# Optimization experiments

Measured on AMD Instinct MI355X. Metric: run time of the kernel, lower is better.

The kernel has to match this reference:

```python
import jax, jax.numpy as jnp
import numpy as np

HIDDEN = 2048
N_HEADS = 16
N_KV_HEADS = 4
HEAD_DIM = HIDDEN // N_HEADS  # 128
N_GROUPS = N_HEADS // N_KV_HEADS  # 4


def rotate_half(x):
    # interleaved rotate: (-x_odd, x_even) interleaved back
    x_even = x[..., ::2]
    x_odd = x[..., 1::2]
    return jnp.stack((-x_odd, x_even), axis=-1).reshape(x.shape)


def setup_inputs() -> dict:
    key = jax.random.key(0)
    ks = jax.random.split(key, 8)
    B, S = 4, 2048
    x = jax.random.normal(ks[0], (B, S, HIDDEN), dtype=jnp.float32)
    # RoPE tables (precomputed cos/sin over max positions)
    inv_freq = 1.0 / (1000000.0 ** (np.arange(0, HEAD_DIM, 2, dtype=np.float32) / HEAD_DIM))
    t = np.arange(S, dtype=np.float32)
    freqs = np.outer(t, inv_freq)  # [S, HEAD_DIM/2]
    emb = np.repeat(freqs, 2, axis=-1)  # interleaved layout [S, HEAD_DIM]
    cos = jnp.asarray(np.cos(emb))
    sin = jnp.asarray(np.sin(emb))
    scale = 0.02
    Wq = jax.random.normal(ks[1], (HIDDEN, N_HEADS * HEAD_DIM), dtype=jnp.float32) * scale
    Wk = jax.random.normal(ks[2], (HIDDEN, N_KV_HEADS * HEAD_DIM), dtype=jnp.float32) * scale
    Wv = jax.random.normal(ks[3], (HIDDEN, N_KV_HEADS * HEAD_DIM), dtype=jnp.float32) * scale
    Wo = jax.random.normal(ks[4], (N_HEADS * HEAD_DIM, HIDDEN), dtype=jnp.float32) * scale
    return {"x": x, "cos": cos, "sin": sin, "Wq": Wq, "Wk": Wk, "Wv": Wv, "Wo": Wo}


def reference(x, cos, sin, Wq, Wk, Wv, Wo):
    B, S, D = x.shape
    q = (x @ Wq).reshape(B, S, N_HEADS, HEAD_DIM).transpose(0, 2, 1, 3)      # [B,H,S,d]
    k = (x @ Wk).reshape(B, S, N_KV_HEADS, HEAD_DIM).transpose(0, 2, 1, 3)   # [B,Hkv,S,d]
    v = (x @ Wv).reshape(B, S, N_KV_HEADS, HEAD_DIM).transpose(0, 2, 1, 3)
    # RoPE: position_ids = arange(S); cos/sin [S,d] -> [1,1,S,d]
    c = cos[:S][None, None, :, :]
    s = sin[:S][None, None, :, :]
    q = q * c + rotate_half(q) * s
    k = k * c + rotate_half(k) * s
    # repeat_kv: [B,Hkv,S,d] -> [B,H,S,d]
    k = jnp.repeat(k, N_GROUPS, axis=1)
    v = jnp.repeat(v, N_GROUPS, axis=1)
    # causal SDPA
    scores = jnp.einsum("bhqd,bhkd->bhqk", q, k) / jnp.sqrt(jnp.float32(HEAD_DIM))
    neg = jnp.finfo(scores.dtype).min
    causal = jnp.triu(jnp.full((S, S), neg, dtype=scores.dtype), k=1)
    scores = scores + causal[None, None]
    attn = jax.nn.softmax(scores.astype(jnp.float32), axis=-1).astype(q.dtype)
    out = jnp.einsum("bhqk,bhkd->bhqd", attn, v)
    out = out.transpose(0, 2, 1, 3).reshape(B, S, N_HEADS * HEAD_DIM)
    return out @ Wo
```

## Files before the change

kernel.cpp:

```cpp
#include <hip/hip_runtime.h>
#include <stdint.h>

#define S_LEN 2048
#define BATCH 4
#define HID   2048
#define HD    128
#define NKV   4
#define MTOT  (BATCH*S_LEN)
#define NQT2  (S_LEN/256)
#define QSCALE 0.08838834764831845f

typedef float    f32x4  __attribute__((ext_vector_type(4)));
typedef __bf16   bf16x8 __attribute__((ext_vector_type(8)));
typedef __bf16   bf16x4 __attribute__((ext_vector_type(4)));
typedef unsigned u32x2  __attribute__((ext_vector_type(2)));

__device__ __forceinline__ void gld16(const void* g, void* l) {
    __builtin_amdgcn_global_load_lds(
        (const __attribute__((address_space(1))) void*)g,
        (__attribute__((address_space(3))) void*)l, 16, 0, 0);
}

__global__ void k_conv_x(const float* __restrict__ in, __bf16* __restrict__ out) {
    int i = blockIdx.x * blockDim.x + threadIdx.x;
    f32x4 a = ((const f32x4*)in)[2 * i];
    f32x4 b = ((const f32x4*)in)[2 * i + 1];
    bf16x8 o;
    o[0] = (__bf16)a[0]; o[1] = (__bf16)a[1]; o[2] = (__bf16)a[2]; o[3] = (__bf16)a[3];
    o[4] = (__bf16)b[0]; o[5] = (__bf16)b[1]; o[6] = (__bf16)b[2]; o[7] = (__bf16)b[3];
    ((bf16x8*)out)[i] = o;
}

__global__ void k_transpose_all(const float* __restrict__ Wq,
                                const float* __restrict__ Wk,
                                const float* __restrict__ Wv,
                                const float* __restrict__ Wo,
                                __bf16* __restrict__ wqt,
                                __bf16* __restrict__ wkvt,
                                __bf16* __restrict__ wot) {
    const int z = blockIdx.z;
    const float* in; __bf16* out; int N;
    if      (z == 0) { in = Wq; out = wqt;  N = 2048; }
    else if (z == 1) { in = Wk; out = wkvt; N = 512;  }
    else if (z == 2) { in = Wv; out = wkvt + (size_t)512 * HID; N = 512; }
    else             { in = Wo; out = wot;  N = 2048; }
    int k0 = blockIdx.x * 64, n0 = blockIdx.y * 64;
    if (n0 >= N) return;
    __shared__ float tile[64][65];
    for (int e = threadIdx.x; e < 4096; e += 256) {
        int r = e >> 6, c = e & 63;
        tile[r][c] = in[(size_t)(k0 + r) * N + n0 + c];
    }
    __syncthreads();
    for (int e = threadIdx.x; e < 4096; e += 256) {
        int r = e >> 6, c = e & 63;
        out[(size_t)(n0 + r) * HID + k0 + c] = (__bf16)tile[c][r];
    }
}

__global__ __launch_bounds__(256) void k_gemm_qkv(const __bf16* __restrict__ A,
                                                  const __bf16* __restrict__ Bt,
                                                  unsigned char* __restrict__ qb8,
                                                  unsigned char* __restrict__ kb8,
                                                  __bf16* __restrict__ vtb,
                                                  const float* __restrict__ cosp,
                                                  const float* __restrict__ sinp) {
    __shared__ __align__(16) char smem[33792];
    __bf16* As = (__bf16*)smem;
    __bf16* Bs = (__bf16*)(smem + 16384);
    const int tid = threadIdx.x, lane = tid & 63, wave = tid >> 6;
    const int wm = wave >> 1, wn = wave & 1;
    const int id = blockIdx.x;
    const int xcd = id & 7, g = id >> 3;
    const int m0 = (xcd * 8 + (g & 7)) * 128;
    const int n0 = (g >> 3) * 128;
    const int lo = lane & 15, hi = lane >> 4;
    f32x4 acc[4][4] = {};

    const int srow = wave * 8 + (lane >> 3);
    const int sp   = lane & 7;

    for (int kt = 0; kt < HID; kt += 64) {
#pragma unroll
        for (int r = 0; r < 4; r++) {
            int row = r * 32 + srow;
            int c = sp ^ (row & 7);
            gld16(A + (size_t)(m0 + row) * HID + kt + c * 8, &As[(r * 32 + wave * 8) * 64]);
        }
#pragma unroll
        for (int r = 0; r < 4; r++) {
            int row = r * 32 + srow;
            int c = sp ^ (row & 7);
            gld16(Bt + (size_t)(n0 + row) * HID + kt + c * 8, &Bs[(r * 32 + wave * 8) * 64]);
        }
        __syncthreads();
#pragma unroll
        for (int ks = 0; ks < 2; ks++) {
            bf16x8 af[4], bfr[4];
#pragma unroll
            for (int mt = 0; mt < 4; mt++) {
                int row = wm * 64 + mt * 16 + lo;
                int pp = (ks * 4 + hi) ^ (row & 7);
                af[mt] = *(const bf16x8*)&As[row * 64 + pp * 8];
            }
#pragma unroll
            for (int nt = 0; nt < 4; nt++) {
                int row = wn * 64 + nt * 16 + lo;
                int pp = (ks * 4 + hi) ^ (row & 7);
                bfr[nt] = *(const bf16x8*)&Bs[row * 64 + pp * 8];
            }
#pragma unroll
            for (int mt = 0; mt < 4; mt++)
#pragma unroll
                for (int nt = 0; nt < 4; nt++)
                    acc[mt][nt] = __builtin_amdgcn_mfma_f32_16x16x32_bf16(
                        af[mt], bfr[nt], acc[mt][nt], 0, 0, 0);
        }
        __syncthreads();
    }

    if (n0 < 2560) {
        __bf16* Cs = (__bf16*)smem;
#pragma unroll
        for (int mt = 0; mt < 4; mt++)
#pragma unroll
            for (int nt = 0; nt < 4; nt++) {
                int rl = wm * 64 + mt * 16 + hi * 4;
                int cl = wn * 64 + nt * 16 + lo;
#pragma unroll
                for (int r = 0; r < 4; r++)
                    Cs[(rl + r) * 132 + cl] = (__bf16)acc[mt][nt][r];
            }
        __syncthreads();

        const int crow = tid >> 4;
        const int cch  = tid & 15;
        const int colg = n0 + cch * 8;
        const bool isQ = n0 < 2048;
        const int d0 = colg & (HD - 1);
#pragma unroll
        for (int rep = 0; rep < 8; rep++) {
            int row = rep * 16 + crow;
            int rowg = m0 + row;
            bf16x8 v = *(const bf16x8*)&Cs[row * 132 + cch * 8];
            float f[8];
#pragma unroll
            for (int j = 0; j < 8; j++) f[j] = (float)v[j];
            {
                int s = rowg & (S_LEN - 1);
                f32x4 c0 = *(const f32x4*)&cosp[s * HD + d0];
                f32x4 c1 = *(const f32x4*)&cosp[s * HD + d0 + 4];
                f32x4 s0 = *(const f32x4*)&sinp[s * HD + d0];
                f32x4 s1 = *(const f32x4*)&sinp[s * HD + d0 + 4];
                float cc[8] = {c0[0], c0[1], c0[2], c0[3], c1[0], c1[1], c1[2], c1[3]};
                float ss[8] = {s0[0], s0[1], s0[2], s0[3], s1[0], s1[1], s1[2], s1[3]};
#pragma unroll
                for (int p = 0; p < 4; p++) {
                    float e0 = f[2 * p], e1 = f[2 * p + 1];
                    f[2 * p]     = e0 * cc[2 * p]     - e1 * ss[2 * p];
                    f[2 * p + 1] = e1 * cc[2 * p + 1] + e0 * ss[2 * p + 1];
                }
            }
            if (isQ) {
#pragma unroll
                for (int j = 0; j < 8; j++) f[j] *= QSCALE;
            }
            int u0 = __builtin_amdgcn_cvt_pk_fp8_f32(f[0], f[1], 0, false);
            u0     = __builtin_amdgcn_cvt_pk_fp8_f32(f[2], f[3], u0, true);
            int u1 = __builtin_amdgcn_cvt_pk_fp8_f32(f[4], f[5], 0, false);
            u1     = __builtin_amdgcn_cvt_pk_fp8_f32(f[6], f[7], u1, true);
            u32x2 pk; pk[0] = (unsigned)u0; pk[1] = (unsigned)u1;
            if (isQ) *(u32x2*)&qb8[(size_t)rowg * HID + colg] = pk;
            else     *(u32x2*)&kb8[(size_t)rowg * 512 + (colg - 2048)] = pk;
        }
    } else {
        __bf16* CsT = (__bf16*)smem;
#pragma unroll
        for (int mt = 0; mt < 4; mt++)
#pragma unroll
            for (int nt = 0; nt < 4; nt++) {
                int cl = wn * 64 + nt * 16 + lo;
                int mrow = wm * 64 + mt * 16 + hi * 4;
                bf16x4 w;
#pragma unroll
                for (int r = 0; r < 4; r++) w[r] = (__bf16)acc[mt][nt][r];
                *(bf16x4*)&CsT[cl * 132 + mrow] = w;
            }
        __syncthreads();

        const int kvh = (n0 - 2560) >> 7;
        const int bb = m0 >> 11;
        const int s0 = m0 & (S_LEN - 1);
        __bf16* dst = vtb + (size_t)(bb * NKV + kvh) * HD * S_LEN;
        const int dloc = tid >> 4;
        const int sch  = tid & 15;
#pragma unroll
        for (int rep = 0; rep < 8; rep++) {
            int d = rep * 16 + dloc;
            bf16x8 v = *(const bf16x8*)&CsT[d * 132 + sch * 8];
            *(bf16x8*)&dst[(size_t)d * S_LEN + s0 + sch * 8] = v;
        }
    }
}

__global__ __launch_bounds__(256) void k_gemm_o(const __bf16* __restrict__ A,
                                                const __bf16* __restrict__ Bt,
                                                float* __restrict__ Cp) {
    __shared__ __bf16 As[128 * 64];
    __shared__ __bf16 Bs[128 * 64];
    const int tid = threadIdx.x, lane = tid & 63, wave = tid >> 6;
    const int wm = wave >> 1, wn = wave & 1;
    const int id = blockIdx.x;
    const int xcd = id & 7, g = id >> 3;
    const int m0 = (xcd * 8 + (g & 7)) * 128;
    const int n0 = (g >> 3) * 128;
    const int lo = lane & 15, hi = lane >> 4;
    f32x4 acc[4][4] = {};

    const int srow = wave * 8 + (lane >> 3);
    const int sp   = lane & 7;

    for (int kt = 0; kt < HID; kt += 64) {
#pragma unroll
        for (int r = 0; r < 4; r++) {
            int row = r * 32 + srow;
            int c = sp ^ (row & 7);
            gld16(A + (size_t)(m0 + row) * HID + kt + c * 8, &As[(r * 32 + wave * 8) * 64]);
        }
#pragma unroll
        for (int r = 0; r < 4; r++) {
            int row = r * 32 + srow;
            int c = sp ^ (row & 7);
            gld16(Bt + (size_t)(n0 + row) * HID + kt + c * 8, &Bs[(r * 32 + wave * 8) * 64]);
        }
        __syncthreads();
#pragma unroll
        for (int ks = 0; ks < 2; ks++) {
            bf16x8 af[4], bfr[4];
#pragma unroll
            for (int mt = 0; mt < 4; mt++) {
                int row = wm * 64 + mt * 16 + lo;
                int pp = (ks * 4 + hi) ^ (row & 7);
                af[mt] = *(const bf16x8*)&As[row * 64 + pp * 8];
            }
#pragma unroll
            for (int nt = 0; nt < 4; nt++) {
                int row = wn * 64 + nt * 16 + lo;
                int pp = (ks * 4 + hi) ^ (row & 7);
                bfr[nt] = *(const bf16x8*)&Bs[row * 64 + pp * 8];
            }
#pragma unroll
            for (int mt = 0; mt < 4; mt++)
#pragma unroll
                for (int nt = 0; nt < 4; nt++)
                    acc[mt][nt] = __builtin_amdgcn_mfma_f32_16x16x32_bf16(
                        af[mt], bfr[nt], acc[mt][nt], 0, 0, 0);
        }
        __syncthreads();
    }
#pragma unroll
    for (int mt = 0; mt < 4; mt++) {
#pragma unroll
        for (int nt = 0; nt < 4; nt++) {
            int row = m0 + wm * 64 + mt * 16 + hi * 4;
            int col = n0 + wn * 64 + nt * 16 + lo;
#pragma unroll
            for (int r = 0; r < 4; r++)
                Cp[(size_t)(row + r) * HID + col] = acc[mt][nt][r];
        }
    }
}

__global__ __launch_bounds__(512) void k_attn(const unsigned char* __restrict__ qb8,
                                              const unsigned char* __restrict__ kb8,
                                              const __bf16* __restrict__ vtb,
                                              __bf16* __restrict__ ob) {
    __shared__ char   Ks8[2][64 * 128];
    __shared__ __bf16 Vs[2][128 * 64];
    __shared__ __bf16 Ps[8][2048];
    const int tid = threadIdx.x, lane = tid & 63, wave = tid >> 6;
    const int pair = blockIdx.x, h = blockIdx.y, b = blockIdx.z;
    const int kvh = h >> 2;
    const int lo = lane & 15, hi = lane >> 4;
    char* PsW = (char*)&Ps[wave][0];

    const unsigned char* kbb = kb8 + (size_t)b * S_LEN * 512 + kvh * HD;
    const __bf16* vbb = vtb + (size_t)(b * NKV + kvh) * HD * S_LEN;

    const int krow_s = tid >> 3;
    const int kp_s   = tid & 7;
    const int vrow_s = wave * 8 + (lane >> 3);
    const int vp_s   = lane & 7;

    auto STAGE_K = [&](int buf, int t) {
        int c = kp_s ^ (krow_s & 7);
        gld16(kbb + (size_t)(t * 64 + krow_s) * 512 + c * 16,
              &Ks8[buf][wave * 1024]);
    };
    auto STAGE_V = [&](int buf, int t) {
#pragma unroll
        for (int r = 0; r < 2; r++) {
            int row = r * 64 + vrow_s;
            int c = vp_s ^ (row & 7);
            gld16(vbb + (size_t)row * S_LEN + t * 64 + c * 8,
                  &Vs[buf][(r * 64 + wave * 8) * 64]);
        }
    };

    auto SM = [&](f32x4 (&sc)[4], float& Mr, float& Lr, f32x4 (&o)[8]) {
        float mloc = sc[0][0];
#pragma unroll
        for (int nt = 0; nt < 4; nt++)
#pragma unroll
            for (int r = 0; r < 4; r++) mloc = fmaxf(mloc, sc[nt][r]);
        mloc = fmaxf(mloc, __shfl_xor(mloc, 16, 64));
        mloc = fmaxf(mloc, __shfl_xor(mloc, 32, 64));
        float mn = (mloc <= Mr + 8.f) ? Mr : mloc;
        float sum = 0.f;
#pragma unroll
        for (int nt = 0; nt < 4; nt++)
#pragma unroll
            for (int r = 0; r < 4; r++) {
                float e = __expf(sc[nt][r] - mn);
                sc[nt][r] = e;
                sum += e;
            }
        sum += __shfl_xor(sum, 16, 64);
        sum += __shfl_xor(sum, 32, 64);
        if (mn != Mr) {
            float scl = __expf(Mr - mn);
            Lr = Lr * scl + sum;
            Mr = mn;
#pragma unroll
            for (int dt = 0; dt < 8; dt++) o[dt] *= scl;
        } else {
            Lr += sum;
        }
    };

#pragma unroll 1
    for (int pi = 0; pi < 2; pi++) {
        const int qt = pi ? (NQT2 - 1 - pair) : pair;
        const int nkv = 4 * qt + 4;
        const int qbase = qt * 256 + wave * 32;

        const unsigned char* qp0 = qb8 + (size_t)(b * S_LEN + qbase + lo) * HID + h * HD;
        const unsigned char* qp1 = qp0 + (size_t)16 * HID;
        long qa0[4], qa1[4];
#pragma unroll
        for (int kf = 0; kf < 4; kf++) {
            qa0[kf] = *(const long*)(qp0 + kf * 32 + hi * 8);
            qa1[kf] = *(const long*)(qp1 + kf * 32 + hi * 8);
        }

        f32x4 o0[8] = {}, o1[8] = {};
        float Mr0 = -3e30f, Lr0 = 0.f, Mr1 = -3e30f, Lr1 = 0.f;

        int cur = 0;
        if (pi == 1) __syncthreads();
        STAGE_K(0, 0);
        STAGE_V(0, 0);
        __syncthreads();

#pragma unroll 1
        for (int t = 0; t < nkv; t++) {
            if (t < nkv - 1) { STAGE_K(cur ^ 1, t + 1); STAGE_V(cur ^ 1, t + 1); }

            f32x4 sc0[4], sc1[4];
            __builtin_amdgcn_s_setprio(1);
#pragma unroll
            for (int nt = 0; nt < 4; nt++) {
                f32x4 a = {0.f, 0.f, 0.f, 0.f}, bb = {0.f, 0.f, 0.f, 0.f};
#pragma unroll
                for (int kf = 0; kf < 4; kf++) {
                    int row = nt * 16 + lo;
                    int lch = 2 * kf + (hi >> 1);
                    long kf8 = *(const long*)&Ks8[cur][row * 128 +
                                ((lch ^ (row & 7)) * 16) + (hi & 1) * 8];
                    a  = __builtin_amdgcn_mfma_f32_16x16x32_fp8_fp8(kf8, qa0[kf], a, 0, 0, 0);
                    bb = __builtin_amdgcn_mfma_f32_16x16x32_fp8_fp8(kf8, qa1[kf], bb, 0, 0, 0);
                }
                sc0[nt] = a; sc1[nt] = bb;
            }
            __builtin_amdgcn_s_setprio(0);

            if (t * 64 + 63 > qbase) {
                int qg = qbase + lo;
#pragma unroll
                for (int nt = 0; nt < 4; nt++)
#pragma unroll
                    for (int r = 0; r < 4; r++) {
                        int kg = t * 64 + nt * 16 + hi * 4 + r;
                        if (kg > qg) sc0[nt][r] = -1e30f;
                    }
            }
            if (t * 64 + 63 > qbase + 16) {
                int qg = qbase + 16 + lo;
#pragma unroll
                for (int nt = 0; nt < 4; nt++)
#pragma unroll
                    for (int r = 0; r < 4; r++) {
                        int kg = t * 64 + nt * 16 + hi * 4 + r;
                        if (kg > qg) sc1[nt][r] = -1e30f;
                    }
            }

            SM(sc0, Mr0, Lr0, o0);
            SM(sc1, Mr1, Lr1, o1);

#pragma unroll
            for (int nt = 0; nt < 4; nt++) {
                bf16x4 p0, p1;
#pragma unroll
                for (int r = 0; r < 4; r++) { p0[r] = (__bf16)sc0[nt][r]; p1[r] = (__bf16)sc1[nt][r]; }
                int off = lo * 128 + ((nt * 32 + hi * 8) ^ ((lo & 7) << 4));
                *(bf16x4*)(PsW + off)        = p0;
                *(bf16x4*)(PsW + 2048 + off) = p1;
            }
            asm volatile("s_waitcnt lgkmcnt(0)" ::: "memory");
            bf16x8 pf0[2], pf1[2];
#pragma unroll
            for (int c = 0; c < 2; c++) {
                int off = lo * 128 + ((c * 64 + hi * 16) ^ ((lo & 7) << 4));
                pf0[c] = *(const bf16x8*)(PsW + off);
                pf1[c] = *(const bf16x8*)(PsW + 2048 + off);
            }
            __builtin_amdgcn_s_setprio(1);
#pragma unroll
            for (int dt = 0; dt < 8; dt++) {
                int rowd = dt * 16 + lo;
#pragma unroll
                for (int c = 0; c < 2; c++) {
                    int ch = c * 4 + hi;
                    bf16x8 vv = *(const bf16x8*)&Vs[cur][rowd * 64 + (ch ^ (rowd & 7)) * 8];
                    o0[dt] = __builtin_amdgcn_mfma_f32_16x16x32_bf16(vv, pf0[c], o0[dt], 0, 0, 0);
                    o1[dt] = __builtin_amdgcn_mfma_f32_16x16x32_bf16(vv, pf1[c], o1[dt], 0, 0, 0);
                }
            }
            __builtin_amdgcn_s_setprio(0);
            __syncthreads();
            cur ^= 1;
        }

        const int qe = lane >> 2, c4 = lane & 3;
#pragma unroll
        for (int sub = 0; sub < 2; sub++) {
            float rl = 1.0f / (sub ? Lr1 : Lr0);
            char* Pp = PsW + sub * 2048;
#pragma unroll
            for (int h2 = 0; h2 < 2; h2++) {
#pragma unroll
                for (int dt4 = 0; dt4 < 4; dt4++) {
                    f32x4 ov = sub ? o1[h2 * 4 + dt4] : o0[h2 * 4 + dt4];
                    bf16x4 w;
#pragma unroll
                    for (int r = 0; r < 4; r++) w[r] = (__bf16)(ov[r] * rl);
                    *(bf16x4*)(Pp + lo * 128 + ((dt4 * 32 + hi * 8) ^ ((lo & 7) << 4))) = w;
                }
                asm volatile("s_waitcnt lgkmcnt(0)" ::: "memory");
                __builtin_amdgcn_sched_barrier(0);
#pragma unroll
                for (int s2 = 0; s2 < 2; s2++) {
                    int ch = c4 + s2 * 4;
                    bf16x8 v = *(const bf16x8*)(Pp + qe * 128 + ((ch * 16) ^ ((qe & 7) << 4)));
                    int qg = qbase + sub * 16 + qe;
                    int col = h * HD + h2 * 64 + ch * 8;
                    *(bf16x8*)&ob[(size_t)(b * S_LEN + qg) * HID + col] = v;
                }
            }
        }
    }
}

extern "C" void kernel_launch(void* const* d_in, const int* in_sizes, int n_in,
                              void* d_out, int out_size, void* d_ws, size_t ws_size,
                              hipStream_t stream) {
    (void)in_sizes; (void)n_in; (void)out_size; (void)ws_size;
    const float* x    = (const float*)d_in[0];
    const float* cosp = (const float*)d_in[1];
    const float* sinp = (const float*)d_in[2];
    const float* Wq   = (const float*)d_in[3];
    const float* Wk   = (const float*)d_in[4];
    const float* Wv   = (const float*)d_in[5];
    const float* Wo   = (const float*)d_in[6];
    float* out = (float*)d_out;

    char* ws = (char*)d_ws;
    __bf16*        xb   = (__bf16*)(ws);
    __bf16*        wqt  = (__bf16*)(ws + 33554432);
    __bf16*        wkvt = (__bf16*)(ws + 41943040);
    __bf16*        wot  = (__bf16*)(ws + 46137344);
    unsigned char* qb8  = (unsigned char*)(ws + 54525952);
    unsigned char* kb8  = (unsigned char*)(ws + 71303168);
    __bf16*        vtb  = (__bf16*)(ws + 75497472);
    __bf16*        aob  = xb;

    k_conv_x<<<MTOT * HID / 8 / 256, 256, 0, stream>>>(x, xb);
    { dim3 g(32, 32, 4);
      k_transpose_all<<<g, 256, 0, stream>>>(Wq, Wk, Wv, Wo, wqt, wkvt, wot); }

    k_gemm_qkv<<<1536, 256, 0, stream>>>(xb, wqt, qb8, kb8, vtb, cosp, sinp);

    { dim3 g(NQT2 / 2, 16, BATCH); k_attn<<<g, 512, 0, stream>>>(qb8, kb8, vtb, aob); }

    k_gemm_o<<<1024, 256, 0, stream>>>(aob, wot, out);
}
```

Measured before the change: 338.2 us.

## Replace output GEMM with 256x256 double-buffered 8-wave ping-pong kernel

New measurement: 327.3 us. 3.2% less time.

```diff
diff --git a/kernel.cpp b/kernel.cpp
--- a/kernel.cpp
+++ b/kernel.cpp
@@ -203,72 +203,132 @@
     }
 }
 
-__global__ __launch_bounds__(256) void k_gemm_o(const __bf16* __restrict__ A,
-                                                const __bf16* __restrict__ Bt,
-                                                float* __restrict__ Cp) {
-    __shared__ __bf16 As[128 * 64];
-    __shared__ __bf16 Bs[128 * 64];
+#define BARM asm volatile("s_barrier" ::: "memory")
+#define BAR1 do { BARM;                                                       \
+                  asm volatile("s_waitcnt lgkmcnt(0)" ::: "memory");          \
+                  __builtin_amdgcn_sched_barrier(0); } while (0)
+#define BAR2 BARM
+#define MM(qm, qn)                                                            \
+    do {                                                                      \
+        __builtin_amdgcn_s_setprio(1);                                        \
+        _Pragma("unroll") for (int ks = 0; ks < 2; ks++)                      \
+        _Pragma("unroll") for (int mf = 0; mf < 4; mf++)                      \
+        _Pragma("unroll") for (int nf = 0; nf < 2; nf++)                      \
+            acc[qm][qn][mf][nf] = __builtin_amdgcn_mfma_f32_16x16x32_bf16(    \
+                af[mf][ks], bf[nf][ks], acc[qm][qn][mf][nf], 0, 0, 0);        \
+        __builtin_amdgcn_s_setprio(0);                                        \
+    } while (0)
+
+__global__ __launch_bounds__(512) void k_gemm_o8(const __bf16* __restrict__ A,
+                                                 const __bf16* __restrict__ Bt,
+                                                 float* __restrict__ Cp) {
+    __shared__ __bf16 Ab[2][2][128 * 64];
+    __shared__ __bf16 Bb[2][2][128 * 64];
     const int tid = threadIdx.x, lane = tid & 63, wave = tid >> 6;
-    const int wm = wave >> 1, wn = wave & 1;
-    const int id = blockIdx.x;
-    const int xcd = id & 7, g = id >> 3;
-    const int m0 = (xcd * 8 + (g & 7)) * 128;
-    const int n0 = (g >> 3) * 128;
+    const int wm = wave >> 2, wn = wave & 3;
+    const int m0 = (blockIdx.x >> 3) * 256;
+    const int n0 = (blockIdx.x & 7) * 256;
     const int lo = lane & 15, hi = lane >> 4;
-    f32x4 acc[4][4] = {};
+    f32x4 acc[2][2][4][2] = {};
 
     const int srow = wave * 8 + (lane >> 3);
     const int sp   = lane & 7;
 
-    for (int kt = 0; kt < HID; kt += 64) {
-#pragma unroll
-        for (int r = 0; r < 4; r++) {
-            int row = r * 32 + srow;
-            int c = sp ^ (row & 7);
-            gld16(A + (size_t)(m0 + row) * HID + kt + c * 8, &As[(r * 32 + wave * 8) * 64]);
-        }
-#pragma unroll
-        for (int r = 0; r < 4; r++) {
-            int row = r * 32 + srow;
-            int c = sp ^ (row & 7);
-            gld16(Bt + (size_t)(n0 + row) * HID + kt + c * 8, &Bs[(r * 32 + wave * 8) * 64]);
-        }
-        __syncthreads();
-#pragma unroll
-        for (int ks = 0; ks < 2; ks++) {
-            bf16x8 af[4], bfr[4];
-#pragma unroll
-            for (int mt = 0; mt < 4; mt++) {
-                int row = wm * 64 + mt * 16 + lo;
-                int pp = (ks * 4 + hi) ^ (row & 7);
-                af[mt] = *(const bf16x8*)&As[row * 64 + pp * 8];
-            }
-#pragma unroll
-            for (int nt = 0; nt < 4; nt++) {
-                int row = wn * 64 + nt * 16 + lo;
-                int pp = (ks * 4 + hi) ^ (row & 7);
-                bfr[nt] = *(const bf16x8*)&Bs[row * 64 + pp * 8];
-            }
-#pragma unroll
-            for (int mt = 0; mt < 4; mt++)
-#pragma unroll
-                for (int nt = 0; nt < 4; nt++)
-                    acc[mt][nt] = __builtin_amdgcn_mfma_f32_16x16x32_bf16(
-                        af[mt], bfr[nt], acc[mt][nt], 0, 0, 0);
-        }
-        __syncthreads();
+    auto STA = [&](int s, int h, int t) {
+#pragma unroll
+        for (int p = 0; p < 2; p++) {
+            int rr = p * 64 + srow;
+            int c = sp ^ (rr & 7);
+            gld16(A + (size_t)(m0 + h * 128 + rr) * HID + t * 64 + c * 8,
+                  &Ab[s][h][(p * 64 + wave * 8) * 64]);
+        }
+    };
+    auto STB = [&](int s, int h, int t) {
+#pragma unroll
+        for (int p = 0; p < 2; p++) {
+            int rr = p * 64 + srow;
+            int c = sp ^ (rr & 7);
+            gld16(Bt + (size_t)(n0 + h * 128 + rr) * HID + t * 64 + c * 8,
+                  &Bb[s][h][(p * 64 + wave * 8) * 64]);
+        }
+    };
+
+    bf16x8 af[4][2], bf[2][2];
+    auto LDA = [&](int s, int qm) {
+#pragma unroll
+        for (int mf = 0; mf < 4; mf++) {
+            int rr = wm * 64 + mf * 16 + lo;
+#pragma unroll
+            for (int ks = 0; ks < 2; ks++) {
+                int pp = (ks * 4 + hi) ^ (rr & 7);
+                af[mf][ks] = *(const bf16x8*)&Ab[s][qm][rr * 64 + pp * 8];
+            }
+        }
+    };
+    auto LDB = [&](int s, int qn) {
+#pragma unroll
+        for (int nf = 0; nf < 2; nf++) {
+            int rr = wn * 32 + nf * 16 + lo;
+#pragma unroll
+            for (int ks = 0; ks < 2; ks++) {
+                int pp = (ks * 4 + hi) ^ (rr & 7);
+                bf[nf][ks] = *(const bf16x8*)&Bb[s][qn][rr * 64 + pp * 8];
+            }
+        }
+    };
+
+    STA(0, 0, 0); STB(0, 0, 0); STA(0, 1, 0); STB(0, 1, 0);
+    STA(1, 1, 1); STB(1, 1, 1);
+    asm volatile("s_waitcnt vmcnt(4)" ::: "memory");
+    BARM;
+
+#pragma unroll 1
+    for (int i = 0; i < 16; i++) {
+        const int t0 = 2 * i, t1 = 2 * i + 1;
+        const bool more = (i < 15);
+        LDA(0, 0); LDB(0, 0);
+        STA(1, 0, t1); STB(1, 0, t1);
+        BAR1; MM(0, 0); BAR2;
+        LDB(0, 1);
+        BAR1; MM(0, 1); BAR2;
+        LDA(0, 1); LDB(0, 0);
+        if (more) STA(0, 0, t0 + 2);
+        BAR1; MM(1, 0); BAR2;
+        LDB(0, 1);
+        if (more) STB(0, 0, t0 + 2);
+        BAR1; MM(1, 1);
+        if (more) { asm volatile("s_waitcnt vmcnt(4)" ::: "memory"); }
+        else      { asm volatile("s_waitcnt vmcnt(0)" ::: "memory"); }
+        BAR2;
+        LDA(1, 1); LDB(1, 1);
+        if (more) { STA(0, 1, t0 + 2); STB(0, 1, t0 + 2); }
+        BAR1; MM(1, 1); BAR2;
+        LDB(1, 0);
+        BAR1; MM(1, 0); BAR2;
+        LDA(1, 0); LDB(1, 1);
+        if (more) STA(1, 1, t1 + 2);
+        BAR1; MM(0, 1); BAR2;
+        LDB(1, 0);
+        if (more) STB(1, 1, t1 + 2);
+        BAR1; MM(0, 0);
+        if (more) { asm volatile("s_waitcnt vmcnt(4)" ::: "memory"); }
+        BAR2;
     }
-#pragma unroll
-    for (int mt = 0; mt < 4; mt++) {
-#pragma unroll
-        for (int nt = 0; nt < 4; nt++) {
-            int row = m0 + wm * 64 + mt * 16 + hi * 4;
-            int col = n0 + wn * 64 + nt * 16 + lo;
-#pragma unroll
-            for (int r = 0; r < 4; r++)
-                Cp[(size_t)(row + r) * HID + col] = acc[mt][nt][r];
-        }
-    }
+
+#pragma unroll
+    for (int qm = 0; qm < 2; qm++)
+#pragma unroll
+        for (int qn = 0; qn < 2; qn++)
+#pragma unroll
+            for (int mf = 0; mf < 4; mf++)
+#pragma unroll
+                for (int nf = 0; nf < 2; nf++) {
+                    int row = m0 + qm * 128 + wm * 64 + mf * 16 + hi * 4;
+                    int col = n0 + qn * 128 + wn * 32 + nf * 16 + lo;
+#pragma unroll
+                    for (int r = 0; r < 4; r++)
+                        Cp[(size_t)(row + r) * HID + col] = acc[qm][qn][mf][nf][r];
+                }
 }
 
 __global__ __launch_bounds__(512) void k_attn(const unsigned char* __restrict__ qb8,
@@ -503,5 +563,5 @@
 
     { dim3 g(NQT2 / 2, 16, BATCH); k_attn<<<g, 512, 0, stream>>>(qb8, kb8, vtb, aob); }
 
-    k_gemm_o<<<1024, 256, 0, stream>>>(aob, wot, out);
-}
+    k_gemm_o8<<<256, 512, 0, stream>>>(aob, wot, out);
+}
```

## Use 256x256 double-buffered ping-pong GEMM for Q and output projections

Applied to the files above, without the earlier changes.

Result: faster. 319.2 us (-5.6%).

```diff
diff --git a/kernel.cpp b/kernel.cpp
--- a/kernel.cpp
+++ b/kernel.cpp
@@ -58,95 +58,140 @@
     }
 }
 
-__global__ __launch_bounds__(256) void k_gemm_qkv(const __bf16* __restrict__ A,
-                                                  const __bf16* __restrict__ Bt,
-                                                  unsigned char* __restrict__ qb8,
-                                                  unsigned char* __restrict__ kb8,
-                                                  __bf16* __restrict__ vtb,
-                                                  const float* __restrict__ cosp,
-                                                  const float* __restrict__ sinp) {
-    __shared__ __align__(16) char smem[33792];
-    __bf16* As = (__bf16*)smem;
-    __bf16* Bs = (__bf16*)(smem + 16384);
-    const int tid = threadIdx.x, lane = tid & 63, wave = tid >> 6;
-    const int wm = wave >> 1, wn = wave & 1;
-    const int id = blockIdx.x;
-    const int xcd = id & 7, g = id >> 3;
-    const int m0 = (xcd * 8 + (g & 7)) * 128;
-    const int n0 = (g >> 3) * 128;
-    const int lo = lane & 15, hi = lane >> 4;
-    f32x4 acc[4][4] = {};
-
-    const int srow = wave * 8 + (lane >> 3);
-    const int sp   = lane & 7;
-
-    for (int kt = 0; kt < HID; kt += 64) {
-#pragma unroll
-        for (int r = 0; r < 4; r++) {
-            int row = r * 32 + srow;
-            int c = sp ^ (row & 7);
-            gld16(A + (size_t)(m0 + row) * HID + kt + c * 8, &As[(r * 32 + wave * 8) * 64]);
-        }
-#pragma unroll
-        for (int r = 0; r < 4; r++) {
-            int row = r * 32 + srow;
-            int c = sp ^ (row & 7);
-            gld16(Bt + (size_t)(n0 + row) * HID + kt + c * 8, &Bs[(r * 32 + wave * 8) * 64]);
-        }
-        __syncthreads();
-#pragma unroll
-        for (int ks = 0; ks < 2; ks++) {
-            bf16x8 af[4], bfr[4];
-#pragma unroll
-            for (int mt = 0; mt < 4; mt++) {
-                int row = wm * 64 + mt * 16 + lo;
-                int pp = (ks * 4 + hi) ^ (row & 7);
-                af[mt] = *(const bf16x8*)&As[row * 64 + pp * 8];
-            }
-#pragma unroll
-            for (int nt = 0; nt < 4; nt++) {
-                int row = wn * 64 + nt * 16 + lo;
-                int pp = (ks * 4 + hi) ^ (row & 7);
-                bfr[nt] = *(const bf16x8*)&Bs[row * 64 + pp * 8];
-            }
-#pragma unroll
-            for (int mt = 0; mt < 4; mt++)
-#pragma unroll
-                for (int nt = 0; nt < 4; nt++)
-                    acc[mt][nt] = __builtin_amdgcn_mfma_f32_16x16x32_bf16(
-                        af[mt], bfr[nt], acc[mt][nt], 0, 0, 0);
-        }
-        __syncthreads();
+#define BARM asm volatile("s_barrier" ::: "memory")
+#define BAR1 do { BARM;                                                       \
+                  asm volatile("s_waitcnt lgkmcnt(0)" ::: "memory");          \
+                  __builtin_amdgcn_sched_barrier(0); } while (0)
+#define BAR2 BARM
+#define MM(qm, qn)                                                            \
+    do {                                                                      \
+        __builtin_amdgcn_s_setprio(1);                                        \
+        _Pragma("unroll") for (int ks = 0; ks < 2; ks++)                      \
+        _Pragma("unroll") for (int mf = 0; mf < 4; mf++)                      \
+        _Pragma("unroll") for (int nf = 0; nf < 2; nf++)                      \
+            acc[qm][qn][mf][nf] = __builtin_amdgcn_mfma_f32_16x16x32_bf16(    \
+                af[mf][ks], bf[nf][ks], acc[qm][qn][mf][nf], 0, 0, 0);        \
+        __builtin_amdgcn_s_setprio(0);                                        \
+    } while (0)
+
+#define GEMM8_BODY(Aptr, Bptr)                                                \
+    __shared__ __bf16 Ab[2][2][128 * 64];                                     \
+    __shared__ __bf16 Bb[2][2][128 * 64];                                     \
+    const int tid = threadIdx.x, lane = tid & 63, wave = tid >> 6;            \
+    const int wm = wave >> 2, wn = wave & 3;                                  \
+    const int lo = lane & 15, hi = lane >> 4;                                 \
+    f32x4 acc[2][2][4][2] = {};                                               \
+    const int srow = wave * 8 + (lane >> 3);                                  \
+    const int sp   = lane & 7;                                                \
+    auto STA = [&](int s, int h, int t) {                                     \
+        _Pragma("unroll") for (int p = 0; p < 2; p++) {                       \
+            int rr = p * 64 + srow;                                           \
+            int c = sp ^ (rr & 7);                                            \
+            gld16(Aptr + (size_t)(m0 + h * 128 + rr) * HID + t * 64 + c * 8,  \
+                  &Ab[s][h][(p * 64 + wave * 8) * 64]);                       \
+        }                                                                     \
+    };                                                                        \
+    auto STB = [&](int s, int h, int t) {                                     \
+        _Pragma("unroll") for (int p = 0; p < 2; p++) {                       \
+            int rr = p * 64 + srow;                                           \
+            int c = sp ^ (rr & 7);                                            \
+            gld16(Bptr + (size_t)(n0 + h * 128 + rr) * HID + t * 64 + c * 8,  \
+                  &Bb[s][h][(p * 64 + wave * 8) * 64]);                       \
+        }                                                                     \
+    };                                                                        \
+    bf16x8 af[4][2], bf[2][2];                                                \
+    auto LDA = [&](int s, int qm) {                                           \
+        _Pragma("unroll") for (int mf = 0; mf < 4; mf++) {                    \
+            int rr = wm * 64 + mf * 16 + lo;                                  \
+            _Pragma("unroll") for (int ks = 0; ks < 2; ks++) {                \
+                int pp = (ks * 4 + hi) ^ (rr & 7);                            \
+                af[mf][ks] = *(const bf16x8*)&Ab[s][qm][rr * 64 + pp * 8];    \
+            }                                                                 \
+        }                                                                     \
+    };                                                                        \
+    auto LDB = [&](int s, int qn) {                                           \
+        _Pragma("unroll") for (int nf = 0; nf < 2; nf++) {                    \
+            int rr = wn * 32 + nf * 16 + lo;                                  \
+            _Pragma("unroll") for (int ks = 0; ks < 2; ks++) {                \
+                int pp = (ks * 4 + hi) ^ (rr & 7);                            \
+                bf[nf][ks] = *(const bf16x8*)&Bb[s][qn][rr * 64 + pp * 8];    \
+            }                                                                 \
+        }                                                                     \
+    };                                                                        \
+    STA(0, 0, 0); STB(0, 0, 0); STA(0, 1, 0); STB(0, 1, 0);                   \
+    STA(1, 1, 1); STB(1, 1, 1);                                               \
+    asm volatile("s_waitcnt vmcnt(4)" ::: "memory");                          \
+    BARM;                                                                     \
+    _Pragma("unroll 1")                                                       \
+    for (int i = 0; i < 16; i++) {                                            \
+        const int t0 = 2 * i, t1 = 2 * i + 1;                                 \
+        const bool more = (i < 15);                                           \
+        LDA(0, 0); LDB(0, 0);                                                 \
+        STA(1, 0, t1); STB(1, 0, t1);                                         \
+        BAR1; MM(0, 0); BAR2;                                                 \
+        LDB(0, 1);                                                            \
+        BAR1; MM(0, 1); BAR2;                                                 \
+        LDA(0, 1); LDB(0, 0);                                                 \
+        if (more) STA(0, 0, t0 + 2);                                          \
+        BAR1; MM(1, 0); BAR2;                                                 \
+        LDB(0, 1);                                                            \
+        if (more) STB(0, 0, t0 + 2);                                          \
+        BAR1; MM(1, 1);                                                       \
+        if (more) { asm volatile("s_waitcnt vmcnt(4)" ::: "memory"); }        \
+        else      { asm volatile("s_waitcnt vmcnt(0)" ::: "memory"); }        \
+        BAR2;                                                                 \
+        LDA(1, 1); LDB(1, 1);                                                 \
+        if (more) { STA(0, 1, t0 + 2); STB(0, 1, t0 + 2); }                   \
+        BAR1; MM(1, 1); BAR2;                                                 \
+        LDB(1, 0);                                                            \
+        BAR1; MM(1, 0); BAR2;                                                 \
+        LDA(1, 0); LDB(1, 1);                                                 \
+        if (more) STA(1, 1, t1 + 2);                                          \
+        BAR1; MM(0, 1); BAR2;                                                 \
+        LDB(1, 0);                                                            \
+        if (more) STB(1, 1, t1 + 2);                                          \
+        BAR1; MM(0, 0);                                                       \
+        if (more) { asm volatile("s_waitcnt vmcnt(4)" ::: "memory"); }        \
+        BAR2;                                                                 \
     }
 
-    if (n0 < 2560) {
-        __bf16* Cs = (__bf16*)smem;
-#pragma unroll
-        for (int mt = 0; mt < 4; mt++)
-#pragma unroll
-            for (int nt = 0; nt < 4; nt++) {
-                int rl = wm * 64 + mt * 16 + hi * 4;
-                int cl = wn * 64 + nt * 16 + lo;
-#pragma unroll
-                for (int r = 0; r < 4; r++)
-                    Cs[(rl + r) * 132 + cl] = (__bf16)acc[mt][nt][r];
-            }
-        __syncthreads();
-
-        const int crow = tid >> 4;
-        const int cch  = tid & 15;
-        const int colg = n0 + cch * 8;
-        const bool isQ = n0 < 2048;
-        const int d0 = colg & (HD - 1);
-#pragma unroll
-        for (int rep = 0; rep < 8; rep++) {
-            int row = rep * 16 + crow;
-            int rowg = m0 + row;
-            bf16x8 v = *(const bf16x8*)&Cs[row * 132 + cch * 8];
-            float f[8];
-#pragma unroll
-            for (int j = 0; j < 8; j++) f[j] = (float)v[j];
-            {
+__global__ __launch_bounds__(512) void k_gemm_q8(const __bf16* __restrict__ A,
+                                                 const __bf16* __restrict__ Bt,
+                                                 unsigned char* __restrict__ qb8,
+                                                 const float* __restrict__ cosp,
+                                                 const float* __restrict__ sinp) {
+    const int m0 = (blockIdx.x >> 3) * 256;
+    const int n0 = (blockIdx.x & 7) * 256;
+    GEMM8_BODY(A, Bt)
+
+    __bf16* Cs = (__bf16*)&Ab[0][0][0];
+    const int crow = tid >> 4;
+    const int cch  = tid & 15;
+    const int d0 = cch * 8;
+#pragma unroll
+    for (int qm = 0; qm < 2; qm++)
+#pragma unroll
+        for (int qn = 0; qn < 2; qn++) {
+#pragma unroll
+            for (int mf = 0; mf < 4; mf++)
+#pragma unroll
+                for (int nf = 0; nf < 2; nf++) {
+                    int rl = wm * 64 + mf * 16 + hi * 4;
+                    int cl = wn * 32 + nf * 16 + lo;
+#pragma unroll
+                    for (int r = 0; r < 4; r++)
+                        Cs[(rl + r) * 132 + cl] = (__bf16)acc[qm][qn][mf][nf][r];
+                }
+            __syncthreads();
+#pragma unroll
+            for (int rep = 0; rep < 4; rep++) {
+                int row = rep * 32 + crow;
+                int rowg = m0 + qm * 128 + row;
+                int colg = n0 + qn * 128 + cch * 8;
+                bf16x8 v = *(const bf16x8*)&Cs[row * 132 + cch * 8];
+                float f[8];
+#pragma unroll
+                for (int j = 0; j < 8; j++) f[j] = (float)v[j];
                 int s = rowg & (S_LEN - 1);
                 f32x4 c0 = *(const f32x4*)&cosp[s * HD + d0];
                 f32x4 c1 = *(const f32x4*)&cosp[s * HD + d0 + 4];
@@ -157,21 +202,146 @@
 #pragma unroll
                 for (int p = 0; p < 4; p++) {
                     float e0 = f[2 * p], e1 = f[2 * p + 1];
-                    f[2 * p]     = e0 * cc[2 * p]     - e1 * ss[2 * p];
-                    f[2 * p + 1] = e1 * cc[2 * p + 1] + e0 * ss[2 * p + 1];
+                    f[2 * p]     = (e0 * cc[2 * p]     - e1 * ss[2 * p])     * QSCALE;
+                    f[2 * p + 1] = (e1 * cc[2 * p + 1] + e0 * ss[2 * p + 1]) * QSCALE;
                 }
-            }
-            if (isQ) {
-#pragma unroll
-                for (int j = 0; j < 8; j++) f[j] *= QSCALE;
+                int u0 = __builtin_amdgcn_cvt_pk_fp8_f32(f[0], f[1], 0, false);
+                u0     = __builtin_amdgcn_cvt_pk_fp8_f32(f[2], f[3], u0, true);
+                int u1 = __builtin_amdgcn_cvt_pk_fp8_f32(f[4], f[5], 0, false);
+                u1     = __builtin_amdgcn_cvt_pk_fp8_f32(f[6], f[7], u1, true);
+                u32x2 pk; pk[0] = (unsigned)u0; pk[1] = (unsigned)u1;
+                *(u32x2*)&qb8[(size_t)rowg * HID + colg] = pk;
+            }
+            __syncthreads();
+        }
+}
+
+__global__ __launch_bounds__(512) void k_gemm_o8(const __bf16* __restrict__ A,
+                                                 const __bf16* __restrict__ Bt,
+                                                 float* __restrict__ Cp) {
+    const int m0 = (blockIdx.x >> 3) * 256;
+    const int n0 = (blockIdx.x & 7) * 256;
+    GEMM8_BODY(A, Bt)
+
+#pragma unroll
+    for (int qm = 0; qm < 2; qm++)
+#pragma unroll
+        for (int qn = 0; qn < 2; qn++)
+#pragma unroll
+            for (int mf = 0; mf < 4; mf++)
+#pragma unroll
+                for (int nf = 0; nf < 2; nf++) {
+                    int row = m0 + qm * 128 + wm * 64 + mf * 16 + hi * 4;
+                    int col = n0 + qn * 128 + wn * 32 + nf * 16 + lo;
+#pragma unroll
+                    for (int r = 0; r < 4; r++)
+                        Cp[(size_t)(row + r) * HID + col] = acc[qm][qn][mf][nf][r];
+                }
+}
+
+__global__ __launch_bounds__(256) void k_gemm_kv(const __bf16* __restrict__ A,
+                                                 const __bf16* __restrict__ Bt,
+                                                 unsigned char* __restrict__ kb8,
+                                                 __bf16* __restrict__ vtb,
+                                                 const float* __restrict__ cosp,
+                                                 const float* __restrict__ sinp) {
+    __shared__ __align__(16) char smem[33792];
+    __bf16* As = (__bf16*)smem;
+    __bf16* Bs = (__bf16*)(smem + 16384);
+    const int tid = threadIdx.x, lane = tid & 63, wave = tid >> 6;
+    const int wm = wave >> 1, wn = wave & 1;
+    const int m0 = blockIdx.x * 128;
+    const int n0 = 2048 + blockIdx.y * 128;
+    const int lo = lane & 15, hi = lane >> 4;
+    f32x4 acc[4][4] = {};
+
+    const int srow = wave * 8 + (lane >> 3);
+    const int sp   = lane & 7;
+
+    for (int kt = 0; kt < HID; kt += 64) {
+#pragma unroll
+        for (int r = 0; r < 4; r++) {
+            int row = r * 32 + srow;
+            int c = sp ^ (row & 7);
+            gld16(A + (size_t)(m0 + row) * HID + kt + c * 8, &As[(r * 32 + wave * 8) * 64]);
+        }
+#pragma unroll
+        for (int r = 0; r < 4; r++) {
+            int row = r * 32 + srow;
+            int c = sp ^ (row & 7);
+            gld16(Bt + (size_t)(n0 + row) * HID + kt + c * 8, &Bs[(r * 32 + wave * 8) * 64]);
+        }
+        __syncthreads();
+#pragma unroll
+        for (int ks = 0; ks < 2; ks++) {
+            bf16x8 af[4], bfr[4];
+#pragma unroll
+            for (int mt = 0; mt < 4; mt++) {
+                int row = wm * 64 + mt * 16 + lo;
+                int pp = (ks * 4 + hi) ^ (row & 7);
+                af[mt] = *(const bf16x8*)&As[row * 64 + pp * 8];
+            }
+#pragma unroll
+            for (int nt = 0; nt < 4; nt++) {
+                int row = wn * 64 + nt * 16 + lo;
+                int pp = (ks * 4 + hi) ^ (row & 7);
+                bfr[nt] = *(const bf16x8*)&Bs[row * 64 + pp * 8];
+            }
+#pragma unroll
+            for (int mt = 0; mt < 4; mt++)
+#pragma unroll
+                for (int nt = 0; nt < 4; nt++)
+                    acc[mt][nt] = __builtin_amdgcn_mfma_f32_16x16x32_bf16(
+                        af[mt], bfr[nt], acc[mt][nt], 0, 0, 0);
+        }
+        __syncthreads();
+    }
+
+    if (n0 < 2560) {
+        __bf16* Cs = (__bf16*)smem;
+#pragma unroll
+        for (int mt = 0; mt < 4; mt++)
+#pragma unroll
+            for (int nt = 0; nt < 4; nt++) {
+                int rl = wm * 64 + mt * 16 + hi * 4;
+                int cl = wn * 64 + nt * 16 + lo;
+#pragma unroll
+                for (int r = 0; r < 4; r++)
+                    Cs[(rl + r) * 132 + cl] = (__bf16)acc[mt][nt][r];
+            }
+        __syncthreads();
+
+        const int crow = tid >> 4;
+        const int cch  = tid & 15;
+        const int colg = n0 + cch * 8;
+        const int d0 = colg & (HD - 1);
+#pragma unroll
+        for (int rep = 0; rep < 8; rep++) {
+            int row = rep * 16 + crow;
+            int rowg = m0 + row;
+            bf16x8 v = *(const bf16x8*)&Cs[row * 132 + cch * 8];
+            float f[8];
+#pragma unroll
+            for (int j = 0; j < 8; j++) f[j] = (float)v[j];
+            int s = rowg & (S_LEN - 1);
+            f32x4 c0 = *(const f32x4*)&cosp[s * HD + d0];
+            f32x4 c1 = *(const f32x4*)&cosp[s * HD + d0 + 4];
+            f32x4 s0 = *(const f32x4*)&sinp[s * HD + d0];
+            f32x4 s1 = *(const f32x4*)&sinp[s * HD + d0 + 4];
+            float cc[8] = {c0[0], c0[1], c0[2], c0[3], c1[0], c1[1], c1[2], c1[3]};
+            float ss[8] = {s0[0], s0[1], s0[2], s0[3], s1[0], s1[1], s1[2], s1[3]};
+#pragma unroll
+            for (int p = 0; p < 4; p++) {
+                float e0 = f[2 * p], e1 = f[2 * p + 1];
+                f[2 * p]     = e0 * cc[2 * p]     - e1 * ss[2 * p];
+                f[2 * p + 1] = e1 * cc[2 * p + 1] + e0 * ss[2 * p + 1];
             }
             int u0 = __builtin_amdgcn_cvt_pk_fp8_f32(f[0], f[1], 0, false);
             u0     = __builtin_amdgcn_cvt_pk_fp8_f32(f[2], f[3], u0, true);
             int u1 = __builtin_amdgcn_cvt_pk_fp8_f32(f[4], f[5], 0, false);
             u1     = __builtin_amdgcn_cvt_pk_fp8_f32(f[6], f[7], u1, true);
             u32x2 pk; pk[0] = (unsigned)u0; pk[1] = (unsigned)u1;
-            if (isQ) *(u32x2*)&qb8[(size_t)rowg * HID + colg] = pk;
-            else     *(u32x2*)&kb8[(size_t)rowg * 512 + (colg - 2048)] = pk;
+            *(u32x2*)&kb8[(size_t)rowg * 512 + (colg - 2048)] = pk;
         }
     } else {
         __bf16* CsT = (__bf16*)smem;
@@ -199,74 +369,6 @@
             int d = rep * 16 + dloc;
             bf16x8 v = *(const bf16x8*)&CsT[d * 132 + sch * 8];
             *(bf16x8*)&dst[(size_t)d * S_LEN + s0 + sch * 8] = v;
-        }
-    }
-}
-
-__global__ __launch_bounds__(256) void k_gemm_o(const __bf16* __restrict__ A,
-                                                const __bf16* __restrict__ Bt,
-                                                float* __restrict__ Cp) {
-    __shared__ __bf16 As[128 * 64];
-    __shared__ __bf16 Bs[128 * 64];
-    const int tid = threadIdx.x, lane = tid & 63, wave = tid >> 6;
-    const int wm = wave >> 1, wn = wave & 1;
-    const int id = blockIdx.x;
-    const int xcd = id & 7, g = id >> 3;
-    const int m0 = (xcd * 8 + (g & 7)) * 128;
-    const int n0 = (g >> 3) * 128;
-    const int lo = lane & 15, hi = lane >> 4;
-    f32x4 acc[4][4] = {};
-
-    const int srow = wave * 8 + (lane >> 3);
-    const int sp   = lane & 7;
-
-    for (int kt = 0; kt < HID; kt += 64) {
-#pragma unroll
-        for (int r = 0; r < 4; r++) {
-            int row = r * 32 + srow;
-            int c = sp ^ (row & 7);
-            gld16(A + (size_t)(m0 + row) * HID + kt + c * 8, &As[(r * 32 + wave * 8) * 64]);
-        }
-#pragma unroll
-        for (int r = 0; r < 4; r++) {
-            int row = r * 32 + srow;
-            int c = sp ^ (row & 7);
-            gld16(Bt + (size_t)(n0 + row) * HID + kt + c * 8, &Bs[(r * 32 + wave * 8) * 64]);
-        }
-        __syncthreads();
-#pragma unroll
-        for (int ks = 0; ks < 2; ks++) {
-            bf16x8 af[4], bfr[4];
-#pragma unroll
-            for (int mt = 0; mt < 4; mt++) {
-                int row = wm * 64 + mt * 16 + lo;
-                int pp = (ks * 4 + hi) ^ (row & 7);
-                af[mt] = *(const bf16x8*)&As[row * 64 + pp * 8];
-            }
-#pragma unroll
-            for (int nt = 0; nt < 4; nt++) {
-                int row = wn * 64 + nt * 16 + lo;
-                int pp = (ks * 4 + hi) ^ (row & 7);
-                bfr[nt] = *(const bf16x8*)&Bs[row * 64 + pp * 8];
-            }
-#pragma unroll
-            for (int mt = 0; mt < 4; mt++)
-#pragma unroll
-                for (int nt = 0; nt < 4; nt++)
-                    acc[mt][nt] = __builtin_amdgcn_mfma_f32_16x16x32_bf16(
-                        af[mt], bfr[nt], acc[mt][nt], 0, 0, 0);
-        }
-        __syncthreads();
-    }
-#pragma unroll
-    for (int mt = 0; mt < 4; mt++) {
-#pragma unroll
-        for (int nt = 0; nt < 4; nt++) {
-            int row = m0 + wm * 64 + mt * 16 + hi * 4;
-            int col = n0 + wn * 64 + nt * 16 + lo;
-#pragma unroll
-            for (int r = 0; r < 4; r++)
-                Cp[(size_t)(row + r) * HID + col] = acc[mt][nt][r];
         }
     }
 }
@@ -499,9 +601,10 @@
     { dim3 g(32, 32, 4);
       k_transpose_all<<<g, 256, 0, stream>>>(Wq, Wk, Wv, Wo, wqt, wkvt, wot); }
 
-    k_gemm_qkv<<<1536, 256, 0, stream>>>(xb, wqt, qb8, kb8, vtb, cosp, sinp);
+    k_gemm_q8<<<256, 512, 0, stream>>>(xb, wqt, qb8, cosp, sinp);
+    { dim3 g(64, 8); k_gemm_kv<<<g, 256, 0, stream>>>(xb, wqt, kb8, vtb, cosp, sinp); }
 
     { dim3 g(NQT2 / 2, 16, BATCH); k_attn<<<g, 512, 0, stream>>>(qb8, kb8, vtb, aob); }
 
-    k_gemm_o<<<1024, 256, 0, stream>>>(aob, wot, out);
-}
+    k_gemm_o8<<<256, 512, 0, stream>>>(aob, wot, out);
+}
```
